# Kernel tuning notes

Measured on AMD Instinct MI355X. Metric: run time of the kernel, lower is better.

Reference implementation:

```python
import jax, jax.numpy as jnp
import numpy as np

B, N, F, K, H = 2, 1024, 64, 8, 4
M1 = K + 1                # 9
M2 = (F - 1) * K + 1      # 505
TEMP = 1.0


def setup_inputs() -> dict:
    key = jax.random.key(0)
    ks = jax.random.split(key, 8)
    x = jax.random.normal(ks[0], (B, N, F), dtype=jnp.float32)
    # Bernoulli(0.05) dense adjacency
    adj = (jax.random.uniform(ks[1], (B, N, N)) < 0.05).astype(jnp.float32)
    mask = jnp.ones((B, N), dtype=jnp.float32)
    Wl = jax.random.normal(ks[2], (F, K * H), dtype=jnp.float32) * 0.05
    bl = jnp.zeros((K * H,), dtype=jnp.float32)
    Wr = jax.random.normal(ks[3], (F, K * H), dtype=jnp.float32) * 0.05
    br = jnp.zeros((K * H,), dtype=jnp.float32)
    # fixed affine layer: y = x @ aff_w + aff_b, aff_w[:, :F] = -I, aff_b[M2] = 1
    aff_w = jnp.zeros((F, M1 * M2), dtype=jnp.float32).at[:, :F].set(-jnp.eye(F, dtype=jnp.float32))
    aff_b = jnp.zeros((M1 * M2,), dtype=jnp.float32).at[M2].set(1.0)
    Wm = jax.random.normal(ks[4], (M1 * M2, F), dtype=jnp.float32) * 0.02
    bm = jnp.zeros((F,), dtype=jnp.float32)
    return dict(x=x, adj=adj, mask=mask, Wl=Wl, bl=bl, Wr=Wr, br=br,
                aff_w=aff_w, aff_b=aff_b, Wm=Wm, bm=bm)


def reference(x, adj, mask, Wl, bl, Wr, br, aff_w, aff_b, Wm, bm):
    # --- multi-head edge attention ---
    x_l = (x @ Wl + bl).reshape(B, N, K, H)   # [B,N,K,H]
    x_r = (x @ Wr + br).reshape(B, N, K, H)
    # scores[b,i,j,n,g] = leaky_relu(x_l[b,j] + x_r[b,i]) / temp
    scores = jax.nn.leaky_relu(x_l[:, None, :, :, :] + x_r[:, :, None, :, :]) / TEMP  # [B,N,N,K,H]
    attn_mask = mask[:, None, :] * mask[:, :, None]                # [B,N,N]
    scores = jnp.where(attn_mask[..., None, None] == 0, -1e9, scores)
    att = jax.nn.softmax(scores, axis=2)                           # softmax over source nodes j
    att = jnp.maximum(att * adj[..., None, None], 1e-6)            # clamp(min=1e-6) STE trick
    att = att / jnp.sum(att, axis=2, keepdims=True)                # renormalize
    # --- attention-weighted neighbor gather ---
    x_h = x.reshape(B, N, H, F // H)
    agg = jnp.einsum('bjgk,bijng->bingk', x_h, att).reshape(B, N, K, F)  # [B,N,K,F]
    # --- fixed affine + FFT log-domain geometric mean ---
    x_aff = (agg @ aff_w + aff_b).reshape(B, N, K, M1, M2)
    x_fft = jnp.fft.fft2(x_aff)                                    # over (M1,M2)
    mag = jnp.exp(jnp.mean(jnp.log(jnp.abs(x_fft) + 1e-6), axis=2))  # [B,N,M1,M2]
    ang = jnp.sum(jnp.angle(x_fft), axis=2)
    x_agg = jnp.fft.ifft2(mag * jnp.exp(1j * ang)).real.reshape(B, N, M1 * M2)
    # --- output MLP + node mask ---
    out = x_agg @ Wm + bm
    return out * mask[..., None]
```

## Files before the change

kernel.cpp:

```cpp
#include <hip/hip_runtime.h>
#include <math.h>

#define NN 1024
#define FD 64
#define CH 32
#define M1D 9
#define M2D 505
#define QH 253
#define THALF 2273
#define KPAD 4608
#define KSPLIT 16
#define KCHUNK 288
#define G1SZ 291456
#define G1KS 8

#define FSQRT(x) __builtin_amdgcn_sqrtf(x)
#define FRCP(x)  __builtin_amdgcn_rcpf(x)

typedef short short8 __attribute__((ext_vector_type(8)));
typedef float f32x4 __attribute__((ext_vector_type(4)));

__device__ __forceinline__ unsigned short f2bf(float x) {
    unsigned int u = __builtin_bit_cast(unsigned int, x);
    return (unsigned short)((u + 0x7FFFu + ((u >> 16) & 1u)) >> 16);
}

#define OFF_WP    1024
#define OFF_SUMX  1056
#define OFF_GMT   1184
#define OFF_XL    148640
#define OFF_XR    214176
#define OFF_AGG   279712
#define OFF_PART  1328288
#define OFF_Y     3425440
#define OFF_WT    8144032
#define OFF_G1P   8176800

__global__ __launch_bounds__(256) void build_tw_kernel(float* __restrict__ T,
                                                       float* __restrict__ Wt,
                                                       float* __restrict__ wp,
                                                       float* __restrict__ sumx) {
    int idx = blockIdx.x * 256 + threadIdx.x;
    if (blockIdx.x == 0) {
        if (threadIdx.x < M1D) {
            float ang = (float)threadIdx.x * (-6.2831853f / 9.0f);
            float s, c; __sincosf(ang, &s, &c);
            wp[2*threadIdx.x] = c; wp[2*threadIdx.x+1] = s;
        }
        if (threadIdx.x >= 64 && threadIdx.x < 192) sumx[threadIdx.x - 64] = 0.f;
    }
    if (idx < 506 * 512) {
        int r = idx >> 9, m2 = idx & 511;
        float v = 0.f;
        if (m2 < M2D) {
            int q = r >> 1;
            int t = (q * m2) % M2D;
            float ang = (float)t * (-6.2831853f / 505.0f);
            float s, c; __sincosf(ang, &s, &c);
            v = (r & 1) ? -s : c;
        }
        T[idx] = v;
    } else if (idx < 506 * 512 + 64 * 512) {
        int i2 = idx - 506 * 512;
        int m = i2 >> 9, col = i2 & 511;
        float v = 0.f;
        if (col < 506) {
            int q = col >> 1;
            int t = (q * m) % M2D;
            float ang = (float)t * (-6.2831853f / 505.0f);
            float s, c; __sincosf(ang, &s, &c);
            v = (col & 1) ? s : c;
        }
        Wt[i2] = v;
    }
}

__global__ __launch_bounds__(64) void proj_kernel(const float* __restrict__ x,
                                                  const float* __restrict__ Wl, const float* __restrict__ bl,
                                                  const float* __restrict__ Wr, const float* __restrict__ br,
                                                  float* __restrict__ xl, float* __restrict__ xr,
                                                  float* __restrict__ sumx) {
    int blk = blockIdx.x, tid = threadIdx.x;
    if (blk >= 2048) {
        int bb = blk - 2048;
        int b = bb >> 4, chunk = bb & 15;
        const float* xb = x + (size_t)b * NN * FD;
        float acc = 0.f;
        int j0 = chunk * 64;
        #pragma unroll 4
        for (int j = j0; j < j0 + 64; j++) acc += xb[j*FD + tid];
        atomicAdd(&sumx[b*FD + tid], acc);
        return;
    }
    int node = blk;
    __shared__ float xrow[FD];
    xrow[tid] = x[(size_t)node*FD + tid];
    __syncthreads();
    int c = tid & 31;
    const float* W = (tid < 32) ? Wl : Wr;
    float acc = (tid < 32) ? bl[c] : br[c];
    #pragma unroll
    for (int f = 0; f < FD; f++) acc += xrow[f] * W[f*CH + c];
    float* dst = (tid < 32) ? xl : xr;
    dst[(size_t)node*CH + c] = acc;
}

__global__ __launch_bounds__(256) void g1_gemm_kernel(const float* __restrict__ T,
                                                      const float* __restrict__ Wm,
                                                      float* __restrict__ G1p) {
    int mt = blockIdx.x, m1 = blockIdx.y, ks = blockIdx.z;
    int tid = threadIdx.x;
    __shared__ float As[64][68];
    __shared__ float Bs[64][64];
    int r0 = mt * 64, k0 = ks * 64;
    const float* Wmb = Wm + (size_t)m1 * M2D * FD;
    float ra[16], rb[16];
    #pragma unroll
    for (int i = 0; i < 16; i++) {
        int l = tid + i*256;
        int r = l >> 6, k = l & 63;
        int rr = r0 + r;
        ra[i] = (rr < 506) ? T[(size_t)rr*512 + k0 + k] : 0.f;
    }
    #pragma unroll
    for (int i = 0; i < 16; i++) {
        int l = tid + i*256;
        int k = l >> 6, f = l & 63;
        int krow = k0 + k;
        rb[i] = (krow < M2D) ? Wmb[(size_t)krow*FD + f] : 0.f;
    }
    #pragma unroll
    for (int i = 0; i < 16; i++) {
        int l = tid + i*256;
        As[l & 63][l >> 6] = ra[i];
    }
    #pragma unroll
    for (int i = 0; i < 16; i++) {
        int l = tid + i*256;
        Bs[l >> 6][l & 63] = rb[i];
    }
    __syncthreads();
    float acc[4][4] = {{0.f}};
    int tm = (tid >> 4) * 4, tf = (tid & 15) * 4;
    #pragma unroll 8
    for (int k = 0; k < 64; k++) {
        float4 a = *(const float4*)&As[k][tm];
        float4 b = *(const float4*)&Bs[k][tf];
        acc[0][0] += a.x*b.x; acc[0][1] += a.x*b.y; acc[0][2] += a.x*b.z; acc[0][3] += a.x*b.w;
        acc[1][0] += a.y*b.x; acc[1][1] += a.y*b.y; acc[1][2] += a.y*b.z; acc[1][3] += a.y*b.w;
        acc[2][0] += a.z*b.x; acc[2][1] += a.z*b.y; acc[2][2] += a.z*b.z; acc[2][3] += a.z*b.w;
        acc[3][0] += a.w*b.x; acc[3][1] += a.w*b.y; acc[3][2] += a.w*b.z; acc[3][3] += a.w*b.w;
    }
    float* G1k = G1p + (size_t)ks * G1SZ;
    #pragma unroll
    for (int i = 0; i < 4; i++) {
        int r = r0 + tm + i;
        if (r >= 506) continue;
        int q = r >> 1, reim = r & 1;
        size_t base = (size_t)(m1*QH + q) * 128;
        #pragma unroll
        for (int j = 0; j < 4; j++)
            G1k[base + (tf + j)*2 + reim] = acc[i][j];
    }
}

__global__ __launch_bounds__(64) void gmat_kernel(const float* __restrict__ G1p,
                                                  const float* __restrict__ wp,
                                                  unsigned short* __restrict__ GmT) {
    int t = blockIdx.x;
    int f = threadIdx.x;
    if (t >= THALF) {
        *(unsigned int*)&GmT[(size_t)f*KPAD + 2*t] = 0u;
        return;
    }
    int p, q;
    if (t < QH) { p = 0; q = t; }
    else { int u = t - QH; p = 1 + u / M2D; q = u % M2D; }
    int qq = (q < QH) ? q : (M2D - q);
    float sgn = (q < QH) ? 1.f : -1.f;
    float gr = 0.f, gi = 0.f;
    #pragma unroll
    for (int m1 = 0; m1 < M1D; m1++) {
        size_t o = ((size_t)(m1*QH + qq)*FD + f)*2;
        float ar = 0.f, ai = 0.f;
        #pragma unroll
        for (int ks = 0; ks < G1KS; ks++) {
            ar += G1p[(size_t)ks*G1SZ + o];
            ai += G1p[(size_t)ks*G1SZ + o + 1];
        }
        ai *= sgn;
        int pm = (p * m1) % M1D;
        float cr = wp[2*pm], ci = -wp[2*pm+1];
        gr += ar*cr - ai*ci;
        gi += ar*ci + ai*cr;
    }
    float scale = (t == 0) ? (1.0f/4545.0f) : (2.0f/4545.0f);
    unsigned int pk = (unsigned int)f2bf(gr*scale) | ((unsigned int)f2bf(-gi*scale) << 16);
    *(unsigned int*)&GmT[(size_t)f*KPAD + 2*t] = pk;
}

__global__ __launch_bounds__(256) void attn_agg_kernel(const float* __restrict__ x,
                                                       const float* __restrict__ adj,
                                                       const float* __restrict__ xl,
                                                       const float* __restrict__ xr,
                                                       const float* __restrict__ sumx,
                                                       float* __restrict__ agg) {
    int node = blockIdx.x;
    int b = node >> 10;
    int tid = threadIdx.x;
    __shared__ float xr_s[CH], Zinv[CH], Sinv[CH];
    __shared__ float red16[16][CH];
    __shared__ int act_list[NN + 8];
    __shared__ int act_n;
    __shared__ float qv2[64][CH];

    if (tid < CH) xr_s[tid] = xr[(size_t)node*CH + tid];
    if (tid == 0) act_n = 0;
    __syncthreads();

    int c = tid & 31, jl = tid >> 5;
    const float* xlb = xl + ((size_t)b << 10) * CH;
    const float* adjrow = adj + (size_t)node * NN;

    int c2 = tid & 15, jl16 = tid >> 4;
    const float2* xlb2 = (const float2*)xlb;
    float xrcx = xr_s[2*c2], xrcy = xr_s[2*c2+1];
    float zx = 0.f, zy = 0.f;
    for (int j0 = jl16; j0 < NN; j0 += 128) {
        float2 sv[8];
        #pragma unroll
        for (int u = 0; u < 8; u++) sv[u] = xlb2[(size_t)(j0 + u*16)*16 + c2];
        #pragma unroll
        for (int u = 0; u < 8; u++) {
            float s0 = sv[u].x + xrcx; s0 = s0 > 0.f ? s0 : 0.01f * s0;
            float s1 = sv[u].y + xrcy; s1 = s1 > 0.f ? s1 : 0.01f * s1;
            zx += __expf(s0); zy += __expf(s1);
        }
    }
    red16[jl16][2*c2]   = zx;
    red16[jl16][2*c2+1] = zy;

    float av[4];
    #pragma unroll
    for (int u = 0; u < 4; u++) av[u] = adjrow[tid + u*256];
    __syncthreads();
    if (tid < CH) {
        float z = 0.f;
        #pragma unroll
        for (int r = 0; r < 16; r++) z += red16[r][tid];
        Zinv[tid] = FRCP(z);
    }
    #pragma unroll
    for (int u = 0; u < 4; u++)
        if (av[u] != 0.f) { int p = atomicAdd(&act_n, 1); act_list[p] = tid + u*256; }
    __syncthreads();
    int nact = act_n;

    int f = tid & 63, n0 = tid >> 6;
    int g = f >> 4;
    int c0 = n0*4 + g, c1 = (n0+4)*4 + g;
    const float* xb = x + ((size_t)b << 10) * FD;
    float acc0 = 0.f, acc1 = 0.f, sacc = 0.f;

    for (int base = 0; base < nact; base += 64) {
        int cnt = min(64, nact - base);
        int cntp = (cnt + 7) & ~7;
        for (int u = tid; u < (cnt << 5); u += 256) {
            int jj = u >> 5, cc = u & 31;
            int j = act_list[base + jj];
            float s = xlb[j*CH + cc] + xr_s[cc];
            s = s > 0.f ? s : 0.01f * s;
            float pv = __expf(s) * Zinv[cc];
            float qq = fmaxf(pv, 1e-6f) - 1e-6f;
            qv2[jj][cc] = qq;
            sacc += qq;
        }
        for (int u = tid + (cnt << 5); u < (cntp << 5); u += 256)
            qv2[u >> 5][u & 31] = 0.f;
        if (tid < cntp - cnt) act_list[base + cnt + tid] = act_list[base];
        __syncthreads();
        for (int jb = 0; jb < cntp; jb += 8) {
            float xv[8];
            #pragma unroll
            for (int u = 0; u < 8; u++) xv[u] = xb[act_list[base + jb + u]*FD + f];
            #pragma unroll
            for (int u = 0; u < 8; u++) {
                acc0 += qv2[jb+u][c0] * xv[u];
                acc1 += qv2[jb+u][c1] * xv[u];
            }
        }
        __syncthreads();
    }
    red16[jl][c] = sacc;
    __syncthreads();
    if (tid < CH) {
        float s = 0.f;
        #pragma unroll
        for (int r = 0; r < 8; r++) s += red16[r][tid];
        Sinv[tid] = FRCP(s + (float)NN * 1e-6f);
    }
    __syncthreads();
    float sx = sumx[b*FD + f] * 1e-6f;
    agg[(size_t)node*512 + n0*FD + f]       = (acc0 + sx) * Sinv[c0];
    agg[(size_t)node*512 + (n0+4)*FD + f]   = (acc1 + sx) * Sinv[c1];
}

__global__ __launch_bounds__(256) void ay_kernel(const float* __restrict__ agg,
                                                 const float* __restrict__ Wt,
                                                 unsigned short* __restrict__ Yb) {
    int slab = blockIdx.x, nt = blockIdx.y;
    int tid = threadIdx.x;
    __shared__ float As2[64][68];
    __shared__ float Bs[64][64];
    int tm = (tid >> 4) * 4, tf = (tid & 15) * 4;
    float ra[16], rb[16];
    #pragma unroll
    for (int i = 0; i < 16; i++) {
        int l = tid + i*256;
        int r = l >> 6, k = l & 63;
        ra[i] = agg[(size_t)(slab*64 + r)*64 + k];
    }
    #pragma unroll
    for (int i = 0; i < 16; i++) {
        int l = tid + i*256;
        int k = l >> 6, cc = l & 63;
        rb[i] = Wt[(size_t)k*512 + nt*64 + cc];
    }
    #pragma unroll
    for (int i = 0; i < 16; i++) { int l = tid + i*256; As2[l & 63][l >> 6] = ra[i]; }
    #pragma unroll
    for (int i = 0; i < 16; i++) { int l = tid + i*256; Bs[l >> 6][l & 63] = rb[i]; }
    __syncthreads();
    float acc[4][4] = {{0.f}};
    #pragma unroll 8
    for (int k = 0; k < 64; k++) {
        float4 a = *(const float4*)&As2[k][tm];
        float4 b = *(const float4*)&Bs[k][tf];
        acc[0][0] += a.x*b.x; acc[0][1] += a.x*b.y; acc[0][2] += a.x*b.z; acc[0][3] += a.x*b.w;
        acc[1][0] += a.y*b.x; acc[1][1] += a.y*b.y; acc[1][2] += a.y*b.z; acc[1][3] += a.y*b.w;
        acc[2][0] += a.z*b.x; acc[2][1] += a.z*b.y; acc[2][2] += a.z*b.z; acc[2][3] += a.z*b.w;
        acc[3][0] += a.w*b.x; acc[3][1] += a.w*b.y; acc[3][2] += a.w*b.z; acc[3][3] += a.w*b.w;
    }
    __syncthreads();
    #pragma unroll
    for (int i = 0; i < 4; i++)
        #pragma unroll
        for (int j = 0; j < 4; j++)
            As2[tm + i][tf + j] = acc[i][j];
    __syncthreads();

    int qloc = tid & 31, node = tid >> 5;
    unsigned short* Yrow = Yb + (size_t)(slab*8 + node)*KPAD;
    int q = nt*32 + qloc;

    if (q <= 252) {
        float2 Av[8];
        #pragma unroll
        for (int n = 0; n < 8; n++)
            Av[n] = make_float2(As2[node*8 + n][2*qloc], As2[node*8 + n][2*qloc + 1]);

        const float CPt[5] = {1.0f, 0.766044443119f, 0.173648177667f, -0.5f, -0.939692620786f};
        const float SPt[5] = {0.0f, -0.642787609687f, -0.984807753012f, -0.866025403784f, -0.342020143326f};

        #define Y_PROD(CSIGN, TIDX)                                            \
        {                                                                      \
            float Pr = 1.f, Pi = 0.f, rp2 = 1.f;                               \
            _Pragma("unroll")                                                  \
            for (int n = 0; n < 8; n++) {                                      \
                float Xr = cp - Av[n].x, Xi = sp - (CSIGN) * Av[n].y;          \
                rp2 *= (Xr*Xr + Xi*Xi);                                        \
                float nPr = Pr*Xr - Pi*Xi;                                     \
                Pi = Pr*Xi + Pi*Xr; Pr = nPr;                                  \
            }                                                                  \
            float pAbs = FSQRT(Pr*Pr + Pi*Pi);                                 \
            float rp8 = FSQRT(FSQRT(FSQRT(FSQRT(rp2))));                       \
            float s = rp8 * FRCP(fmaxf(pAbs, 1e-20f));                         \
            unsigned int pk = (unsigned int)f2bf(s*Pr) | ((unsigned int)f2bf(s*Pi) << 16); \
            *(unsigned int*)&Yrow[2*(TIDX)] = pk;                              \
        }

        #pragma unroll
        for (int p = 0; p < 5; p++) {
            float cp = CPt[p], sp = SPt[p];
            int tfwd = (p == 0) ? q : (QH + (p-1)*M2D + q);
            Y_PROD(1.f, tfwd);
            if (p >= 1 && q >= 1) {
                int tmir = QH + (p-1)*M2D + (M2D - q);
                Y_PROD(-1.f, tmir);
            }
        }
        #undef Y_PROD
    }
    if (nt == 7 && tid < 248) {
        int rr = tid / 31, cc2 = tid % 31;
        unsigned short* Yr2 = Yb + (size_t)(slab*8 + rr)*KPAD;
        *(unsigned int*)&Yr2[2*THALF + 2*cc2] = 0u;
    }
}

__global__ __launch_bounds__(256) void gemm_kernel(const unsigned short* __restrict__ Yb,
                                                   const unsigned short* __restrict__ GmT,
                                                   float* __restrict__ part) {
    int mtile = blockIdx.x, kc = blockIdx.y;
    int tid = threadIdx.x;
    __shared__ unsigned short Ys[64*40];
    __shared__ unsigned short Gs[64*40];
    int m0 = mtile * 64;
    int k0 = kc * KCHUNK;
    int r = tid >> 2, kg = (tid & 3) * 8;
    const unsigned short* Ysrc = Yb + (size_t)(m0 + r)*KPAD + k0 + kg;
    const unsigned short* Gsrc = GmT + (size_t)r*KPAD + k0 + kg;
    uint4 ya = *(const uint4*)Ysrc;
    uint4 ga = *(const uint4*)Gsrc;
    int w = tid >> 6, lane = tid & 63;
    int lm = lane & 15, quad = lane >> 4;
    f32x4 acc0 = {0.f,0.f,0.f,0.f}, acc1 = acc0, acc2 = acc0, acc3 = acc0;
    for (int ks = 0; ks < KCHUNK; ks += 32) {
        *(uint4*)&Ys[r*40 + kg] = ya;
        *(uint4*)&Gs[r*40 + kg] = ga;
        __syncthreads();
        if (ks + 32 < KCHUNK) {
            ya = *(const uint4*)(Ysrc + ks + 32);
            ga = *(const uint4*)(Gsrc + ks + 32);
        }
        short8 b  = *(const short8*)&Gs[(w*16 + lm)*40 + quad*8];
        short8 a0 = *(const short8*)&Ys[(lm)*40      + quad*8];
        short8 a1 = *(const short8*)&Ys[(16 + lm)*40 + quad*8];
        short8 a2 = *(const short8*)&Ys[(32 + lm)*40 + quad*8];
        short8 a3 = *(const short8*)&Ys[(48 + lm)*40 + quad*8];
        acc0 = __builtin_amdgcn_mfma_f32_16x16x32_bf16(a0, b, acc0, 0, 0, 0);
        acc1 = __builtin_amdgcn_mfma_f32_16x16x32_bf16(a1, b, acc1, 0, 0, 0);
        acc2 = __builtin_amdgcn_mfma_f32_16x16x32_bf16(a2, b, acc2, 0, 0, 0);
        acc3 = __builtin_amdgcn_mfma_f32_16x16x32_bf16(a3, b, acc3, 0, 0, 0);
        __syncthreads();
    }
    float* prow = part + (size_t)kc * (2048*FD);
    int col = w*16 + lm;
    #pragma unroll
    for (int rr = 0; rr < 4; rr++) {
        int row = quad*4 + rr;
        prow[(size_t)(m0 + row)*FD + col]      = acc0[rr];
        prow[(size_t)(m0 + 16 + row)*FD + col] = acc1[rr];
        prow[(size_t)(m0 + 32 + row)*FD + col] = acc2[rr];
        prow[(size_t)(m0 + 48 + row)*FD + col] = acc3[rr];
    }
}

__global__ __launch_bounds__(256) void reduce_kernel(const float* __restrict__ part,
                                                     const float* __restrict__ bm,
                                                     const float* __restrict__ mask,
                                                     float* __restrict__ out) {
    int idx = blockIdx.x * 256 + threadIdx.x;
    if (idx >= 32768) return;
    const float4* p4 = (const float4*)part;
    float4 s = p4[idx];
    #pragma unroll
    for (int kc = 1; kc < KSPLIT; kc++) {
        float4 v = p4[(size_t)kc*32768 + idx];
        s.x += v.x; s.y += v.y; s.z += v.z; s.w += v.w;
    }
    int f0 = (idx & 15) * 4;
    int node = idx >> 4;
    float mk = mask[node];
    s.x = (s.x + bm[f0])   * mk;
    s.y = (s.y + bm[f0+1]) * mk;
    s.z = (s.z + bm[f0+2]) * mk;
    s.w = (s.w + bm[f0+3]) * mk;
    ((float4*)out)[idx] = s;
}

extern "C" void kernel_launch(void* const* d_in, const int* in_sizes, int n_in,
                              void* d_out, int out_size, void* d_ws, size_t ws_size,
                              hipStream_t stream) {
    const float* x    = (const float*)d_in[0];
    const float* adj  = (const float*)d_in[1];
    const float* mask = (const float*)d_in[2];
    const float* Wl   = (const float*)d_in[3];
    const float* bl   = (const float*)d_in[4];
    const float* Wr   = (const float*)d_in[5];
    const float* br   = (const float*)d_in[6];
    const float* Wm   = (const float*)d_in[9];
    const float* bm   = (const float*)d_in[10];
    float* out = (float*)d_out;
    float* ws  = (float*)d_ws;

    float* wp   = ws + OFF_WP;
    float* sumx = ws + OFF_SUMX;
    unsigned short* GmT = (unsigned short*)(ws + OFF_GMT);
    float* xl   = ws + OFF_XL;
    float* xr   = ws + OFF_XR;
    float* agg  = ws + OFF_AGG;
    float* part = ws + OFF_PART;
    float* T    = ws + OFF_Y;
    unsigned short* Yb = (unsigned short*)(ws + OFF_Y);
    float* Wt   = ws + OFF_WT;
    float* G1p  = ws + OFF_G1P;

    hipLaunchKernelGGL(build_tw_kernel, dim3((506*512 + 64*512 + 255)/256), dim3(256), 0, stream, T, Wt, wp, sumx);
    hipLaunchKernelGGL(proj_kernel, dim3(2080), dim3(64), 0, stream, x, Wl, bl, Wr, br, xl, xr, sumx);
    hipLaunchKernelGGL(g1_gemm_kernel, dim3(8, 9, G1KS), dim3(256), 0, stream, T, Wm, G1p);
    hipLaunchKernelGGL(gmat_kernel, dim3(KPAD/2), dim3(64), 0, stream, G1p, wp, GmT);
    hipLaunchKernelGGL(attn_agg_kernel, dim3(2048), dim3(256), 0, stream, x, adj, xl, xr, sumx, agg);
    hipLaunchKernelGGL(ay_kernel, dim3(256, 8), dim3(256), 0, stream, agg, Wt, Yb);
    hipLaunchKernelGGL(gemm_kernel, dim3(32, KSPLIT), dim3(256), 0, stream, Yb, GmT, part);
    hipLaunchKernelGGL(reduce_kernel, dim3(128), dim3(256), 0, stream, part, bm, mask, out);
}
```

Before: 177.8 us.

## Merge prep kernels, widen gmat blocks, use log/exp2 for product scaling

Folds the twiddle-table build, projection and column-sum kernels into one launch and replaces the atomic-based sum with a per-batch serial reduction, which removes one launch and the zeroing dependency. The gmat kernel now packs four output columns per 256-thread block instead of one per 64-thread block. In the Y product, the four nested square roots plus reciprocal are replaced by exp2/log2 and rsq intrinsics. The risks are that the two sum blocks now each read a whole batch serially, and that the log/exp path may differ slightly in precision.

```diff
diff --git a/kernel.cpp b/kernel.cpp
--- a/kernel.cpp
+++ b/kernel.cpp
@@ -16,6 +16,9 @@
 
 #define FSQRT(x) __builtin_amdgcn_sqrtf(x)
 #define FRCP(x)  __builtin_amdgcn_rcpf(x)
+#define FRSQ(x)  __builtin_amdgcn_rsqf(x)
+#define FLOG2(x) __builtin_amdgcn_logf(x)
+#define FEXP2(x) __builtin_amdgcn_exp2f(x)
 
 typedef short short8 __attribute__((ext_vector_type(8)));
 typedef float f32x4 __attribute__((ext_vector_type(4)));
@@ -36,19 +39,47 @@
 #define OFF_WT    8144032
 #define OFF_G1P   8176800
 
-__global__ __launch_bounds__(256) void build_tw_kernel(float* __restrict__ T,
-                                                       float* __restrict__ Wt,
-                                                       float* __restrict__ wp,
-                                                       float* __restrict__ sumx) {
-    int idx = blockIdx.x * 256 + threadIdx.x;
-    if (blockIdx.x == 0) {
-        if (threadIdx.x < M1D) {
-            float ang = (float)threadIdx.x * (-6.2831853f / 9.0f);
+__global__ __launch_bounds__(64) void prep_kernel(const float* __restrict__ x,
+                                                  const float* __restrict__ Wl, const float* __restrict__ bl,
+                                                  const float* __restrict__ Wr, const float* __restrict__ br,
+                                                  float* __restrict__ xl, float* __restrict__ xr,
+                                                  float* __restrict__ sumx, float* __restrict__ wp,
+                                                  float* __restrict__ T, float* __restrict__ Wt) {
+    int blk = blockIdx.x, tid = threadIdx.x;
+    if (blk < 2048) {
+        int node = blk;
+        __shared__ float xrow[FD];
+        xrow[tid] = x[(size_t)node*FD + tid];
+        __syncthreads();
+        int c = tid & 31;
+        const float* W = (tid < 32) ? Wl : Wr;
+        float acc = (tid < 32) ? bl[c] : br[c];
+        #pragma unroll
+        for (int f = 0; f < FD; f++) acc += xrow[f] * W[f*CH + c];
+        float* dst = (tid < 32) ? xl : xr;
+        dst[(size_t)node*CH + c] = acc;
+        return;
+    }
+    if (blk < 2050) {
+        int b = blk - 2048;
+        if (b == 0 && tid < M1D) {
+            float ang = (float)tid * (-6.2831853f / 9.0f);
             float s, c; __sincosf(ang, &s, &c);
-            wp[2*threadIdx.x] = c; wp[2*threadIdx.x+1] = s;
-        }
-        if (threadIdx.x >= 64 && threadIdx.x < 192) sumx[threadIdx.x - 64] = 0.f;
-    }
+            wp[2*tid] = c; wp[2*tid+1] = s;
+        }
+        const float* xb = x + (size_t)b * NN * FD;
+        float acc = 0.f;
+        for (int j0 = 0; j0 < NN; j0 += 8) {
+            float v[8];
+            #pragma unroll
+            for (int u = 0; u < 8; u++) v[u] = xb[(j0 + u)*FD + tid];
+            #pragma unroll
+            for (int u = 0; u < 8; u++) acc += v[u];
+        }
+        sumx[b*FD + tid] = acc;
+        return;
+    }
+    int idx = (blk - 2050) * 64 + tid;
     if (idx < 506 * 512) {
         int r = idx >> 9, m2 = idx & 511;
         float v = 0.f;
@@ -60,7 +91,7 @@
             v = (r & 1) ? -s : c;
         }
         T[idx] = v;
-    } else if (idx < 506 * 512 + 64 * 512) {
+    } else {
         int i2 = idx - 506 * 512;
         int m = i2 >> 9, col = i2 & 511;
         float v = 0.f;
@@ -73,36 +104,6 @@
         }
         Wt[i2] = v;
     }
-}
-
-__global__ __launch_bounds__(64) void proj_kernel(const float* __restrict__ x,
-                                                  const float* __restrict__ Wl, const float* __restrict__ bl,
-                                                  const float* __restrict__ Wr, const float* __restrict__ br,
-                                                  float* __restrict__ xl, float* __restrict__ xr,
-                                                  float* __restrict__ sumx) {
-    int blk = blockIdx.x, tid = threadIdx.x;
-    if (blk >= 2048) {
-        int bb = blk - 2048;
-        int b = bb >> 4, chunk = bb & 15;
-        const float* xb = x + (size_t)b * NN * FD;
-        float acc = 0.f;
-        int j0 = chunk * 64;
-        #pragma unroll 4
-        for (int j = j0; j < j0 + 64; j++) acc += xb[j*FD + tid];
-        atomicAdd(&sumx[b*FD + tid], acc);
-        return;
-    }
-    int node = blk;
-    __shared__ float xrow[FD];
-    xrow[tid] = x[(size_t)node*FD + tid];
-    __syncthreads();
-    int c = tid & 31;
-    const float* W = (tid < 32) ? Wl : Wr;
-    float acc = (tid < 32) ? bl[c] : br[c];
-    #pragma unroll
-    for (int f = 0; f < FD; f++) acc += xrow[f] * W[f*CH + c];
-    float* dst = (tid < 32) ? xl : xr;
-    dst[(size_t)node*CH + c] = acc;
 }
 
 __global__ __launch_bounds__(256) void g1_gemm_kernel(const float* __restrict__ T,
@@ -164,11 +165,11 @@
     }
 }
 
-__global__ __launch_bounds__(64) void gmat_kernel(const float* __restrict__ G1p,
-                                                  const float* __restrict__ wp,
-                                                  unsigned short* __restrict__ GmT) {
-    int t = blockIdx.x;
-    int f = threadIdx.x;
+__global__ __launch_bounds__(256) void gmat_kernel(const float* __restrict__ G1p,
+                                                   const float* __restrict__ wp,
+                                                   unsigned short* __restrict__ GmT) {
+    int t = blockIdx.x * 4 + (threadIdx.x >> 6);
+    int f = threadIdx.x & 63;
     if (t >= THALF) {
         *(unsigned int*)&GmT[(size_t)f*KPAD + 2*t] = 0u;
         return;
@@ -372,9 +373,8 @@
                 float nPr = Pr*Xr - Pi*Xi;                                     \
                 Pi = Pr*Xi + Pi*Xr; Pr = nPr;                                  \
             }                                                                  \
-            float pAbs = FSQRT(Pr*Pr + Pi*Pi);                                 \
-            float rp8 = FSQRT(FSQRT(FSQRT(FSQRT(rp2))));                       \
-            float s = rp8 * FRCP(fmaxf(pAbs, 1e-20f));                         \
+            float pp = fmaxf(Pr*Pr + Pi*Pi, 1e-38f);                           \
+            float s = FEXP2(0.0625f * FLOG2(fmaxf(rp2, 1e-38f))) * FRSQ(pp);   \
             unsigned int pk = (unsigned int)f2bf(s*Pr) | ((unsigned int)f2bf(s*Pi) << 16); \
             *(unsigned int*)&Yrow[2*(TIDX)] = pk;                              \
         }
@@ -496,10 +496,10 @@
     float* Wt   = ws + OFF_WT;
     float* G1p  = ws + OFF_G1P;
 
-    hipLaunchKernelGGL(build_tw_kernel, dim3((506*512 + 64*512 + 255)/256), dim3(256), 0, stream, T, Wt, wp, sumx);
-    hipLaunchKernelGGL(proj_kernel, dim3(2080), dim3(64), 0, stream, x, Wl, bl, Wr, br, xl, xr, sumx);
+    hipLaunchKernelGGL(prep_kernel, dim3(6610), dim3(64), 0, stream,
+                       x, Wl, bl, Wr, br, xl, xr, sumx, wp, T, Wt);
     hipLaunchKernelGGL(g1_gemm_kernel, dim3(8, 9, G1KS), dim3(256), 0, stream, T, Wm, G1p);
-    hipLaunchKernelGGL(gmat_kernel, dim3(KPAD/2), dim3(64), 0, stream, G1p, wp, GmT);
+    hipLaunchKernelGGL(gmat_kernel, dim3(576), dim3(256), 0, stream, G1p, wp, GmT);
     hipLaunchKernelGGL(attn_agg_kernel, dim3(2048), dim3(256), 0, stream, x, adj, xl, xr, sumx, agg);
     hipLaunchKernelGGL(ay_kernel, dim3(256, 8), dim3(256), 0, stream, agg, Wt, Yb);
     hipLaunchKernelGGL(gemm_kernel, dim3(32, KSPLIT), dim3(256), 0, stream, Yb, GmT, part);
```

New measurement: 192.1 us. 8.1% more time.
